# Optimization experiments

Measured on AMD Instinct MI355X. Metric: run time of the kernel, lower is better.

## Reference

```python
import jax, jax.numpy as jnp
import numpy as np

D_IN = 512
D_OUT = 512
NUM_HEADS = 8
HEAD_DIM = D_OUT // NUM_HEADS


def setup_inputs() -> dict:
    key = jax.random.key(0)
    ks = jax.random.split(key, 6)
    b, t, n = 4, 32, 256
    scale = 1.0 / np.sqrt(D_IN)
    return {
        "x": jax.random.normal(ks[0], (b, t, n, D_IN), dtype=jnp.float32),
        "Wq": jax.random.normal(ks[1], (D_IN, D_OUT), dtype=jnp.float32) * scale,
        "Wk": jax.random.normal(ks[2], (D_IN, D_OUT), dtype=jnp.float32) * scale,
        "Wv": jax.random.normal(ks[3], (D_IN, D_OUT), dtype=jnp.float32) * scale,
        "Wo": jax.random.normal(ks[4], (D_OUT, D_OUT), dtype=jnp.float32) * scale,
        "bo": jax.random.normal(ks[5], (D_OUT,), dtype=jnp.float32) * 0.01,
    }


def reference(x, Wq, Wk, Wv, Wo, bo):
    b, t, n, _ = x.shape
    h, hd = NUM_HEADS, HEAD_DIM
    # QKV projections (no bias, qkv_bias=False)
    q = (x @ Wq).reshape(b, t, n, h, hd)
    k = (x @ Wk).reshape(b, t, n, h, hd)
    v = (x @ Wv).reshape(b, t, n, h, hd)
    # attention over tokens, per (batch, timestamp, head)
    scores = jnp.einsum('btqhd,btkhd->bthqk', q, k) / np.sqrt(hd).astype(jnp.float32)
    weights = jax.nn.softmax(scores, axis=-1)
    # dropout p=0.0 (eval / deterministic reference) -> identity
    ctx = jnp.einsum('bthqk,btkhd->btqhd', weights, v).reshape(b, t, n, D_OUT)
    return ctx @ Wo + bo
```

## Files before the change

kernel.cpp:

```cpp
#include <hip/hip_runtime.h>
#include <hip/hip_bf16.h>

typedef __attribute__((ext_vector_type(8))) short bf16x8;
typedef __attribute__((ext_vector_type(4))) float f32x4;

#define MFMA_16x16x32(a,b,c) __builtin_amdgcn_mfma_f32_16x16x32_bf16((a),(b),(c),0,0,0)

__device__ __forceinline__ unsigned short f2bf(float f){
  unsigned int u = __float_as_uint(f);
  u += 0x7FFFu + ((u >> 16) & 1u);
  return (unsigned short)(u >> 16);
}

__device__ __forceinline__ unsigned int cvtpk_bf16(float lo, float hi){
  unsigned int r;
  asm("v_cvt_pk_bf16_f32 %0, %1, %2" : "=v"(r) : "v"(lo), "v"(hi));
  return r;
}

__device__ __forceinline__ void async16(const void* g, void* l){
  __builtin_amdgcn_global_load_lds((const __attribute__((address_space(1))) void*)g,
                                   (__attribute__((address_space(3))) void*)l,
                                   16, 0, 0);
}

__global__ __launch_bounds__(256) void convert_x_kernel(const float* __restrict__ x,
                                                        unsigned short* __restrict__ xb, int n4){
  int idx = blockIdx.x*256 + threadIdx.x;
  int stride = gridDim.x*256;
  for (int i = idx; i < n4; i += stride){
    float4 v = reinterpret_cast<const float4*>(x)[i];
    ushort4 o;
    o.x = f2bf(v.x); o.y = f2bf(v.y); o.z = f2bf(v.z); o.w = f2bf(v.w);
    reinterpret_cast<ushort4*>(xb)[i] = o;
  }
}

__global__ __launch_bounds__(256) void prep_weights(const float* __restrict__ Wq,
                                                    const float* __restrict__ Wk,
                                                    const float* __restrict__ Wv,
                                                    const float* __restrict__ Wo,
                                                    unsigned short* __restrict__ WqkvT,
                                                    unsigned short* __restrict__ WoT){
  int idx = blockIdx.x*256 + threadIdx.x;
  int stride = gridDim.x*256;
  const int T1 = 1536*512;
  const int total = T1 + 512*512;
  for (int o = idx; o < total; o += stride){
    if (o < T1){
      int n = o >> 9, k = o & 511;
      const float* W = (n < 512) ? Wq : ((n < 1024) ? Wk : Wv);
      WqkvT[o] = f2bf(W[k*512 + (n & 511)]);
    } else {
      int o2 = o - T1;
      int n = o2 >> 9, k = o2 & 511;
      WoT[o2] = f2bf(Wo[k*512 + n]);
    }
  }
}

template<bool BIAS, bool OUTBF16>
__global__ __launch_bounds__(256) void gemm_bt(const unsigned short* __restrict__ A,
                                               const unsigned short* __restrict__ Bt,
                                               float* __restrict__ Cf, unsigned short* __restrict__ Cb,
                                               const float* __restrict__ bias,
                                               int M, int N, int K, int ldc){
  __shared__ __attribute__((aligned(16))) unsigned short As[128*64];
  __shared__ __attribute__((aligned(16))) unsigned short Bs[128*64];
  const int tid = threadIdx.x;
  const int lane = tid & 63;
  const int w = tid >> 6;
  const int l15 = lane & 15, lhi = lane >> 4;
  const int NB = N >> 7;
  const int bm = blockIdx.x / NB;
  const int bn = blockIdx.x % NB;
  const int wr = w >> 1, wc = w & 1;
  const f32x4 fzero = {0.f,0.f,0.f,0.f};

  f32x4 acc[4][4];
  #pragma unroll
  for (int a=0;a<4;++a)
    #pragma unroll
    for (int b=0;b<4;++b) acc[a][b] = fzero;

  for (int kt = 0; kt < K; kt += 64){
    #pragma unroll
    for (int j=0;j<4;++j){
      int c = (w*4+j)*64 + lane;
      int row = c >> 3;
      int src = ((c & 7) << 4) ^ ((row & 7) << 4);
      async16((const char*)(A + (size_t)(bm*128 + row)*K + kt) + src,
              (char*)As + ((w*4+j) << 10));
    }
    #pragma unroll
    for (int j=0;j<4;++j){
      int c = (w*4+j)*64 + lane;
      int row = c >> 3;
      int src = ((c & 7) << 4) ^ ((row & 7) << 4);
      async16((const char*)(Bt + (size_t)(bn*128 + row)*K + kt) + src,
              (char*)Bs + ((w*4+j) << 10));
    }
    __syncthreads();
    #pragma unroll
    for (int kk=0;kk<2;++kk){
      bf16x8 af[4], bfr[4];
      #pragma unroll
      for (int mi=0;mi<4;++mi){
        int m = wr*64 + mi*16 + l15;
        int off = m*128 + (((kk<<6) + (lhi<<4)) ^ ((m & 7) << 4));
        af[mi] = *reinterpret_cast<const bf16x8*>((const char*)As + off);
      }
      #pragma unroll
      for (int ni=0;ni<4;++ni){
        int n = wc*64 + ni*16 + l15;
        int off = n*128 + (((kk<<6) + (lhi<<4)) ^ ((n & 7) << 4));
        bfr[ni] = *reinterpret_cast<const bf16x8*>((const char*)Bs + off);
      }
      #pragma unroll
      for (int mi=0;mi<4;++mi)
        #pragma unroll
        for (int ni=0;ni<4;++ni)
          acc[mi][ni] = MFMA_16x16x32(af[mi], bfr[ni], acc[mi][ni]);
    }
    __syncthreads();
  }
  #pragma unroll
  for (int mi=0;mi<4;++mi){
    int r = bm*128 + wr*64 + mi*16 + lhi*4;
    #pragma unroll
    for (int ni=0;ni<4;++ni){
      int cc = bn*128 + wc*64 + ni*16 + l15;
      float bv = 0.f;
      if (BIAS) bv = bias[cc];
      #pragma unroll
      for (int i=0;i<4;++i){
        float v = acc[mi][ni][i] + bv;
        if (OUTBF16) Cb[(size_t)(r+i)*ldc + cc] = f2bf(v);
        else         Cf[(size_t)(r+i)*ldc + cc] = v;
      }
    }
  }
}

__global__ __launch_bounds__(256) void attn_kernel(const unsigned short* __restrict__ qkv,
                                                   unsigned short* __restrict__ ctx){
  __shared__ __attribute__((aligned(16))) unsigned short Ks[256*64];
  __shared__ __attribute__((aligned(16))) unsigned short Vst[64*264];

  const int bid = blockIdx.x;
  const int h = bid & 7, bt = bid >> 3;
  const int r0 = bt << 8;
  const int tid = threadIdx.x;
  const int lane = tid & 63, w = tid >> 6;
  const int l15 = lane & 15, lhi = lane >> 4;
  const char* qkvB = (const char*)qkv;
  const f32x4 fzero = {0.f,0.f,0.f,0.f};

  bf16x8 qf[4][2];
  #pragma unroll
  for (int st=0; st<4; ++st){
    int q0 = w*64 + st*16;
    #pragma unroll
    for (int kk=0; kk<2; ++kk)
      qf[st][kk] = *reinterpret_cast<const bf16x8*>(
          qkvB + ((size_t)(r0 + q0 + l15)*1536 + h*64 + kk*32 + lhi*8)*2);
  }

  #pragma unroll
  for (int j=0;j<8;++j){
    int c = (w*8+j)*64 + lane;
    int tok = c >> 3;
    int src = ((c & 7) << 4) ^ ((tok & 7) << 4);
    async16(qkvB + ((size_t)(r0 + tok)*1536 + 512 + h*64)*2 + src,
            (char*)Ks + ((w*8+j) << 10));
  }
  {
    const char* vbase = qkvB + ((size_t)(r0 + tid)*1536 + 1024 + h*64)*2;
    #pragma unroll
    for (int j=0;j<8;++j){
      bf16x8 vv = *reinterpret_cast<const bf16x8*>(vbase + (j<<4));
      #pragma unroll
      for (int e=0;e<8;++e)
        Vst[(j*8+e)*264 + tid] = (unsigned short)vv[e];
    }
  }
  __syncthreads();

  const int ga2 = (lhi & 1) << 1;
  const int lA = l15 + (ga2 << 4);
  const int lB = lA + 16;
  const bool odd = (lhi >> 1) != 0;

  #pragma unroll
  for (int st=0; st<4; ++st){
    const int q0 = w*64 + st*16;

    f32x4 S[16];
    #pragma unroll
    for (int t=0;t<16;++t) S[t] = fzero;
    #pragma unroll
    for (int kk=0;kk<2;++kk){
      #pragma unroll
      for (int t=0;t<16;++t){
        int tok = t*16 + l15;
        int off = tok*128 + (((kk<<6) + (lhi<<4)) ^ ((tok & 7) << 4));
        bf16x8 kf = *reinterpret_cast<const bf16x8*>((const char*)Ks + off);
        S[t] = MFMA_16x16x32(kf, qf[st][kk], S[t]);
      }
    }

    float m = S[0][0];
    #pragma unroll
    for (int t=0;t<16;++t)
      #pragma unroll
      for (int i=0;i<4;++i) m = fmaxf(m, S[t][i]);
    m = fmaxf(m, __shfl_xor(m, 16));
    m = fmaxf(m, __shfl_xor(m, 32));

    float l = 0.f;
    unsigned int P2[32];
    #pragma unroll
    for (int t=0;t<16;++t){
      float p0 = __expf((S[t][0] - m) * 0.125f);
      float p1 = __expf((S[t][1] - m) * 0.125f);
      float p2 = __expf((S[t][2] - m) * 0.125f);
      float p3 = __expf((S[t][3] - m) * 0.125f);
      l += (p0 + p1) + (p2 + p3);
      P2[2*t]   = cvtpk_bf16(p0, p1);
      P2[2*t+1] = cvtpk_bf16(p2, p3);
    }
    l += __shfl_xor(l, 16);
    l += __shfl_xor(l, 32);
    float rl = 1.0f / l;

    f32x4 O[4];
    #pragma unroll
    for (int dt=0;dt<4;++dt) O[dt] = fzero;
    #pragma unroll
    for (int s=0;s<8;++s){
      unsigned int a0e = __shfl((int)P2[4*s+0], lA), a0o = __shfl((int)P2[4*s+2], lA);
      unsigned int a1e = __shfl((int)P2[4*s+1], lA), a1o = __shfl((int)P2[4*s+3], lA);
      unsigned int b0e = __shfl((int)P2[4*s+0], lB), b0o = __shfl((int)P2[4*s+2], lB);
      unsigned int b1e = __shfl((int)P2[4*s+1], lB), b1o = __shfl((int)P2[4*s+3], lB);
      unsigned int u0 = odd ? a0o : a0e;
      unsigned int u1 = odd ? a1o : a1e;
      unsigned int u2 = odd ? b0o : b0e;
      unsigned int u3 = odd ? b1o : b1e;
      bf16x8 pa;
      reinterpret_cast<unsigned int*>(&pa)[0] = u0;
      reinterpret_cast<unsigned int*>(&pa)[1] = u1;
      reinterpret_cast<unsigned int*>(&pa)[2] = u2;
      reinterpret_cast<unsigned int*>(&pa)[3] = u3;
      #pragma unroll
      for (int dt=0;dt<4;++dt){
        bf16x8 vb = *reinterpret_cast<const bf16x8*>(&Vst[(dt*16 + l15)*264 + s*32 + 8*lhi]);
        O[dt] = MFMA_16x16x32(pa, vb, O[dt]);
      }
    }

    float rl4[4];
    #pragma unroll
    for (int i=0;i<4;++i) rl4[i] = __shfl(rl, lhi*4 + i);
    #pragma unroll
    for (int dt=0;dt<4;++dt){
      int col = h*64 + dt*16 + l15;
      #pragma unroll
      for (int i=0;i<4;++i){
        int row = r0 + q0 + lhi*4 + i;
        ctx[(size_t)row*512 + col] = f2bf(O[dt][i] * rl4[i]);
      }
    }
  }
}

extern "C" void kernel_launch(void* const* d_in, const int* in_sizes, int n_in,
                              void* d_out, int out_size, void* d_ws, size_t ws_size,
                              hipStream_t stream) {
  const float* x  = (const float*)d_in[0];
  const float* Wq = (const float*)d_in[1];
  const float* Wk = (const float*)d_in[2];
  const float* Wv = (const float*)d_in[3];
  const float* Wo = (const float*)d_in[4];
  const float* bo = (const float*)d_in[5];
  float* out = (float*)d_out;

  char* ws = (char*)d_ws;
  unsigned short* xb    = (unsigned short*)ws;
  unsigned short* qkv   = (unsigned short*)(ws + 33554432);
  unsigned short* WqkvT = (unsigned short*)(ws + 134217728);
  unsigned short* WoT   = (unsigned short*)(ws + 135790592);
  unsigned short* ctx   = xb;

  convert_x_kernel<<<2048, 256, 0, stream>>>(x, xb, 16777216/4);
  prep_weights<<<1024, 256, 0, stream>>>(Wq, Wk, Wv, Wo, WqkvT, WoT);
  gemm_bt<false, true><<<256*12, 256, 0, stream>>>(xb, WqkvT, nullptr, qkv, nullptr,
                                                   32768, 1536, 512, 1536);
  attn_kernel<<<1024, 256, 0, stream>>>(qkv, ctx);
  gemm_bt<true, false><<<256*4, 256, 0, stream>>>(ctx, WoT, out, nullptr, bo,
                                                  32768, 512, 512, 512);
}
```

Before: 187.9 us.

## Rewrite projection GEMMs as 256x256-tile, 8-wave, double-buffered pipelined kernel

Replaces the 128x128 single-buffered GEMM with a 256x256-tile kernel using 8 waves, double-buffered LDS, and async global-to-LDS loads that are interleaved with MFMA quarter-blocks under fine-grained barriers and s_setprio. The block index is remapped so that neighbouring tiles are spread across XCDs. The aim is to hide load latency behind compute and cut global traffic through larger tile reuse. In exchange it uses 128KB of LDS and far more accumulator registers, and it launches fewer blocks: 256 for the output projection, which may underfill the GPU.

Result: faster. 168.4 us (-10.4%).

```diff
diff --git a/kernel.cpp b/kernel.cpp
--- a/kernel.cpp
+++ b/kernel.cpp
@@ -23,6 +23,9 @@
                                    (__attribute__((address_space(3))) void*)l,
                                    16, 0, 0);
 }
+
+#define FENCE asm volatile("" ::: "memory")
+#define BARR  do{ FENCE; __builtin_amdgcn_s_barrier(); FENCE; }while(0)
 
 __global__ __launch_bounds__(256) void convert_x_kernel(const float* __restrict__ x,
                                                         unsigned short* __restrict__ xb, int n4){
@@ -60,76 +63,97 @@
 }
 
 template<bool BIAS, bool OUTBF16>
-__global__ __launch_bounds__(256) void gemm_bt(const unsigned short* __restrict__ A,
-                                               const unsigned short* __restrict__ Bt,
-                                               float* __restrict__ Cf, unsigned short* __restrict__ Cb,
-                                               const float* __restrict__ bias,
-                                               int M, int N, int K, int ldc){
-  __shared__ __attribute__((aligned(16))) unsigned short As[128*64];
-  __shared__ __attribute__((aligned(16))) unsigned short Bs[128*64];
+__global__ __launch_bounds__(512, 2) void gemm8(const unsigned short* __restrict__ A,
+                                                const unsigned short* __restrict__ Bt,
+                                                float* __restrict__ Cf, unsigned short* __restrict__ Cb,
+                                                const float* __restrict__ bias,
+                                                int K, int NB, int ldc){
+  __shared__ __attribute__((aligned(16))) char ldsA[2][32768];
+  __shared__ __attribute__((aligned(16))) char ldsB[2][32768];
   const int tid = threadIdx.x;
-  const int lane = tid & 63;
-  const int w = tid >> 6;
+  const int lane = tid & 63, w = tid >> 6;
+  const int wr = w >> 2, wc = w & 3;
   const int l15 = lane & 15, lhi = lane >> 4;
-  const int NB = N >> 7;
-  const int bm = blockIdx.x / NB;
-  const int bn = blockIdx.x % NB;
-  const int wr = w >> 1, wc = w & 1;
+  const int xorv = (l15 & 7) << 4;
+
+  const int cpx = gridDim.x >> 3;
+  const int bid = (blockIdx.x & 7) * cpx + (blockIdx.x >> 3);
+  const int bm = bid / NB, bn = bid % NB;
+
+  const int row0 = tid >> 3;
+  const int srcb = ((tid & 7) << 4) ^ ((row0 & 7) << 4);
+  const size_t rK2 = (size_t)K * 2;
+  const char* Ab = (const char*)(A + (size_t)(bm*256 + row0) * K) + srcb;
+  const char* Bb = (const char*)(Bt + (size_t)(bn*256 + row0) * K) + srcb;
+
+#define STG_A(p,h,kt) do{ \
+    async16(Ab + (size_t)((h)*128)*rK2      + (size_t)(kt)*2, ldsA[p] + (h)*16384 +        w*1024); \
+    async16(Ab + (size_t)((h)*128 + 64)*rK2 + (size_t)(kt)*2, ldsA[p] + (h)*16384 + 8192 + w*1024); }while(0)
+#define STG_B(p,h,kt) do{ \
+    async16(Bb + (size_t)((h)*128)*rK2      + (size_t)(kt)*2, ldsB[p] + (h)*16384 +        w*1024); \
+    async16(Bb + (size_t)((h)*128 + 64)*rK2 + (size_t)(kt)*2, ldsB[p] + (h)*16384 + 8192 + w*1024); }while(0)
+
+#define LDAF(p, mh) do{ _Pragma("unroll") for (int f=0;f<4;++f){ \
+    const char* base_ = ldsA[p] + (wr*128 + ((mh)*4+f)*16 + l15)*128; \
+    af[f][0] = *reinterpret_cast<const bf16x8*>(base_ + (((lhi<<4))      ^ xorv)); \
+    af[f][1] = *reinterpret_cast<const bf16x8*>(base_ + ((64 + (lhi<<4)) ^ xorv)); } }while(0)
+#define LDBF(dst, p, nh) do{ _Pragma("unroll") for (int n2=0;n2<2;++n2){ \
+    const char* base_ = ldsB[p] + (wc*64 + ((nh)*2+n2)*16 + l15)*128; \
+    dst[n2][0] = *reinterpret_cast<const bf16x8*>(base_ + (((lhi<<4))      ^ xorv)); \
+    dst[n2][1] = *reinterpret_cast<const bf16x8*>(base_ + ((64 + (lhi<<4)) ^ xorv)); } }while(0)
+#define MFQ(mh, nh, B_) do{ _Pragma("unroll") for (int f=0;f<4;++f) \
+    _Pragma("unroll") for (int n2=0;n2<2;++n2) \
+    _Pragma("unroll") for (int kk=0;kk<2;++kk) \
+      acc[(mh)*4+f][(nh)*2+n2] = MFMA_16x16x32(af[f][kk], B_[n2][kk], acc[(mh)*4+f][(nh)*2+n2]); }while(0)
+
+  f32x4 acc[8][4];
   const f32x4 fzero = {0.f,0.f,0.f,0.f};
-
-  f32x4 acc[4][4];
-  #pragma unroll
-  for (int a=0;a<4;++a)
-    #pragma unroll
-    for (int b=0;b<4;++b) acc[a][b] = fzero;
-
-  for (int kt = 0; kt < K; kt += 64){
-    #pragma unroll
-    for (int j=0;j<4;++j){
-      int c = (w*4+j)*64 + lane;
-      int row = c >> 3;
-      int src = ((c & 7) << 4) ^ ((row & 7) << 4);
-      async16((const char*)(A + (size_t)(bm*128 + row)*K + kt) + src,
-              (char*)As + ((w*4+j) << 10));
-    }
-    #pragma unroll
-    for (int j=0;j<4;++j){
-      int c = (w*4+j)*64 + lane;
-      int row = c >> 3;
-      int src = ((c & 7) << 4) ^ ((row & 7) << 4);
-      async16((const char*)(Bt + (size_t)(bn*128 + row)*K + kt) + src,
-              (char*)Bs + ((w*4+j) << 10));
-    }
-    __syncthreads();
-    #pragma unroll
-    for (int kk=0;kk<2;++kk){
-      bf16x8 af[4], bfr[4];
-      #pragma unroll
-      for (int mi=0;mi<4;++mi){
-        int m = wr*64 + mi*16 + l15;
-        int off = m*128 + (((kk<<6) + (lhi<<4)) ^ ((m & 7) << 4));
-        af[mi] = *reinterpret_cast<const bf16x8*>((const char*)As + off);
-      }
-      #pragma unroll
-      for (int ni=0;ni<4;++ni){
-        int n = wc*64 + ni*16 + l15;
-        int off = n*128 + (((kk<<6) + (lhi<<4)) ^ ((n & 7) << 4));
-        bfr[ni] = *reinterpret_cast<const bf16x8*>((const char*)Bs + off);
-      }
-      #pragma unroll
-      for (int mi=0;mi<4;++mi)
-        #pragma unroll
-        for (int ni=0;ni<4;++ni)
-          acc[mi][ni] = MFMA_16x16x32(af[mi], bfr[ni], acc[mi][ni]);
-    }
-    __syncthreads();
-  }
-  #pragma unroll
-  for (int mi=0;mi<4;++mi){
-    int r = bm*128 + wr*64 + mi*16 + lhi*4;
+  #pragma unroll
+  for (int i=0;i<8;++i)
+    #pragma unroll
+    for (int j=0;j<4;++j) acc[i][j] = fzero;
+  bf16x8 af[4][2], bf0[2][2], bfc[2][2];
+  const int nt = K >> 6;
+
+  STG_B(0,0,0);  STG_B(0,1,0);  STG_A(0,0,0);  STG_A(0,1,0);
+  STG_B(1,0,64); STG_B(1,1,64);
+  asm volatile("s_waitcnt vmcnt(4)" ::: "memory");
+  __builtin_amdgcn_s_barrier(); FENCE;
+
+  for (int t = 0; t < nt; ++t){
+    const int p = t & 1, o = p ^ 1;
+    const int kt1 = (t+1) << 6, kt2 = (t+2) << 6;
+    LDAF(p, 0); LDBF(bf0, p, 0);
+    if (t+1 < nt) STG_A(o, 0, kt1);
+    BARR;
+    __builtin_amdgcn_s_setprio(1); MFQ(0, 0, bf0); __builtin_amdgcn_s_setprio(0);
+    BARR;
+    LDBF(bfc, p, 1);
+    if (t+1 < nt) STG_A(o, 1, kt1);
+    BARR;
+    __builtin_amdgcn_s_setprio(1); MFQ(0, 1, bfc); __builtin_amdgcn_s_setprio(0);
+    BARR;
+    LDAF(p, 1);
+    if (t+2 < nt) STG_B(p, 0, kt2);
+    BARR;
+    __builtin_amdgcn_s_setprio(1); MFQ(1, 1, bfc); __builtin_amdgcn_s_setprio(0);
+    BARR;
+    if (t+2 < nt) STG_B(p, 1, kt2);
+    BARR;
+    __builtin_amdgcn_s_setprio(1); MFQ(1, 0, bf0); __builtin_amdgcn_s_setprio(0);
+    if (t+1 < nt){
+      if (t+2 < nt) asm volatile("s_waitcnt vmcnt(4)" ::: "memory");
+      else          asm volatile("s_waitcnt vmcnt(0)" ::: "memory");
+      __builtin_amdgcn_s_barrier(); FENCE;
+    }
+  }
+
+  #pragma unroll
+  for (int mi=0;mi<8;++mi){
+    const int r = bm*256 + wr*128 + mi*16 + lhi*4;
     #pragma unroll
     for (int ni=0;ni<4;++ni){
-      int cc = bn*128 + wc*64 + ni*16 + l15;
+      const int cc = bn*256 + wc*64 + ni*16 + l15;
       float bv = 0.f;
       if (BIAS) bv = bias[cc];
       #pragma unroll
@@ -140,6 +164,11 @@
       }
     }
   }
+#undef STG_A
+#undef STG_B
+#undef LDAF
+#undef LDBF
+#undef MFQ
 }
 
 __global__ __launch_bounds__(256) void attn_kernel(const unsigned short* __restrict__ qkv,
@@ -293,9 +322,7 @@
 
   convert_x_kernel<<<2048, 256, 0, stream>>>(x, xb, 16777216/4);
   prep_weights<<<1024, 256, 0, stream>>>(Wq, Wk, Wv, Wo, WqkvT, WoT);
-  gemm_bt<false, true><<<256*12, 256, 0, stream>>>(xb, WqkvT, nullptr, qkv, nullptr,
-                                                   32768, 1536, 512, 1536);
+  gemm8<false, true><<<768, 512, 0, stream>>>(xb, WqkvT, nullptr, qkv, nullptr, 512, 6, 1536);
   attn_kernel<<<1024, 256, 0, stream>>>(qkv, ctx);
-  gemm_bt<true, false><<<256*4, 256, 0, stream>>>(ctx, WoT, out, nullptr, bo,
-                                                  32768, 512, 512, 512);
-}
+  gemm8<true, false><<<256, 512, 0, stream>>>(ctx, WoT, out, nullptr, bo, 512, 2, 512);
+}
```
